# Kernel tuning notes

Hardware: AMD Instinct MI355X
Metric: run time of the kernel (lower is better)

Reference implementation:

```python
import jax, jax.numpy as jnp
import numpy as np

B, S, D, H = 4, 2048, 1024, 16
DK = D // H
DFF = 4 * D
EPS = 1e-6


def setup_inputs() -> dict:
    key = jax.random.key(0)
    ks = jax.random.split(key, 16)
    s = 0.02
    return {
        "x": jax.random.normal(ks[0], (B, S, D), jnp.float32),
        "mask": jax.random.randint(ks[1], (B, 1, 1, S), 0, 2, jnp.int32),
        "wq": jax.random.normal(ks[2], (D, D), jnp.float32) * s,
        "bq": jnp.zeros((D,), jnp.float32),
        "wk": jax.random.normal(ks[3], (D, D), jnp.float32) * s,
        "bk": jnp.zeros((D,), jnp.float32),
        "wv": jax.random.normal(ks[4], (D, D), jnp.float32) * s,
        "bv": jnp.zeros((D,), jnp.float32),
        "wo": jax.random.normal(ks[5], (D, D), jnp.float32) * s,
        "bo": jnp.zeros((D,), jnp.float32),
        "w1": jax.random.normal(ks[6], (DFF, D), jnp.float32) * s,
        "b1": jnp.zeros((DFF,), jnp.float32),
        "w2": jax.random.normal(ks[7], (D, DFF), jnp.float32) * s,
        "b2": jnp.zeros((D,), jnp.float32),
        "a1": jnp.ones((1,), jnp.float32),
        "c1": jnp.zeros((1,), jnp.float32),
        "a2": jnp.ones((1,), jnp.float32),
        "c2": jnp.zeros((1,), jnp.float32),
    }


def _layernorm(x, alpha, bias):
    # source: alpha * (x - mean) / (std + eps) + bias, torch std is unbiased
    mean = jnp.mean(x, axis=-1, keepdims=True)
    std = jnp.std(x, axis=-1, keepdims=True, ddof=1)
    return alpha * (x - mean) / (std + EPS) + bias


def _mha(x, mask, wq, bq, wk, bk, wv, bv, wo, bo):
    q = (x @ wq.T + bq).reshape(B, S, H, DK).transpose(0, 2, 1, 3)  # [B,H,S,DK]
    k = (x @ wk.T + bk).reshape(B, S, H, DK).transpose(0, 2, 1, 3)
    v = (x @ wv.T + bv).reshape(B, S, H, DK).transpose(0, 2, 1, 3)
    scores = jnp.einsum("bhqd,bhkd->bhqk", q, k) / jnp.sqrt(jnp.float32(DK))
    scores = jnp.where(mask == 0, jnp.float32(-1e9), scores)
    attn = jax.nn.softmax(scores, axis=-1)
    out = jnp.einsum("bhqk,bhkd->bhqd", attn, v)  # [B,H,S,DK]
    out = out.transpose(0, 2, 1, 3).reshape(B, S, D)
    return out @ wo.T + bo


def reference(x, mask, wq, bq, wk, bk, wv, bv, wo, bo, w1, b1, w2, b2, a1, c1, a2, c2):
    # residual 1: x + MHA(LN(x))  (dropout = identity in eval)
    h = x + _mha(_layernorm(x, a1, c1), mask, wq, bq, wk, bk, wv, bv, wo, bo)
    # residual 2: h + FFN(LN(h))
    hn = _layernorm(h, a2, c2)
    ffn = jax.nn.relu(hn @ w1.T + b1) @ w2.T + b2
    return h + ffn
```

## Files before the change

kernel.cpp:

```cpp
#include <hip/hip_runtime.h>
#include <math.h>

static constexpr int B  = 4;
static constexpr int S  = 2048;
static constexpr int D  = 1024;
static constexpr int H  = 16;
static constexpr int DFF = 4096;

typedef __attribute__((ext_vector_type(8))) short short8;
typedef __attribute__((ext_vector_type(8))) unsigned short ushort8;
typedef __attribute__((ext_vector_type(4))) unsigned short ushort4v;
typedef __attribute__((ext_vector_type(4))) float f32x4;

__device__ __forceinline__ float b2f(unsigned short u) {
  unsigned int x = ((unsigned int)u) << 16;
  float f;
  __builtin_memcpy(&f, &x, 4);
  return f;
}
__device__ __forceinline__ unsigned short f2b(float f) {
  unsigned int x;
  __builtin_memcpy(&x, &f, 4);
  x += 0x7fffu + ((x >> 16) & 1u);
  return (unsigned short)(x >> 16);
}

__device__ __forceinline__ f32x4 mfma16(short8 a, short8 b, f32x4 c) {
  return __builtin_amdgcn_mfma_f32_16x16x32_bf16(a, b, c, 0, 0, 0);
}

__device__ __forceinline__ void gload_lds16(const void* gsrc, void* ldst) {
  __builtin_amdgcn_global_load_lds(
      (__attribute__((address_space(1))) void*)(uintptr_t)gsrc,
      (__attribute__((address_space(3))) void*)ldst, 16, 0, 0);
}

#define LGK0 asm volatile("s_waitcnt lgkmcnt(0)" ::: "memory")
#define VMC8 asm volatile("s_waitcnt vmcnt(8)" ::: "memory")
#define VMC0 asm volatile("s_waitcnt vmcnt(0)" ::: "memory")
#define SB0  __builtin_amdgcn_sched_barrier(0)
#define BAR  __builtin_amdgcn_s_barrier()
#define PRIO1 __builtin_amdgcn_s_setprio(1)
#define PRIO0 __builtin_amdgcn_s_setprio(0)

struct CvtArgs {
  const float* s[6];
  unsigned short* d[6];
  int n[6];
};
__global__ __launch_bounds__(256) void convert6(CvtArgs a) {
  const int seg = blockIdx.y;
  const int i = (blockIdx.x * 256 + threadIdx.x) * 4;
  if (i < a.n[seg]) {
    f32x4 v = *(const f32x4*)(a.s[seg] + i);
    ushort4v o;
#pragma unroll
    for (int j = 0; j < 4; j++) o[j] = f2b(v[j]);
    *(ushort4v*)(a.d[seg] + i) = o;
  }
}

__global__ __launch_bounds__(256) void ln_fused(const float* __restrict__ x,
                                                const float* __restrict__ ap,
                                                const float* __restrict__ cp,
                                                unsigned short* __restrict__ out) {
  const int row = blockIdx.x, tid = threadIdx.x;
  const size_t base = (size_t)row * D;
  float v[4];
  float s = 0.f, sq = 0.f;
#pragma unroll
  for (int i = 0; i < 4; i++) {
    v[i] = x[base + tid + i * 256];
    s += v[i];
    sq += v[i] * v[i];
  }
#pragma unroll
  for (int o = 32; o > 0; o >>= 1) {
    s += __shfl_xor(s, o);
    sq += __shfl_xor(sq, o);
  }
  __shared__ __align__(16) float rs[4], rq[4];
  const int wave = tid >> 6, lane = tid & 63;
  if (lane == 0) {
    rs[wave] = s;
    rq[wave] = sq;
  }
  __syncthreads();
  const float S1 = rs[0] + rs[1] + rs[2] + rs[3];
  const float S2 = rq[0] + rq[1] + rq[2] + rq[3];
  const float mean = S1 * (1.f / 1024.f);
  const float var = fmaxf(0.f, (S2 - 1024.f * mean * mean) * (1.f / 1023.f));
  const float rstd = 1.f / (sqrtf(var) + 1e-6f);
  const float alpha = ap[0], beta = cp[0];
#pragma unroll
  for (int i = 0; i < 4; i++)
    out[base + tid + i * 256] = f2b(alpha * (v[i] - mean) * rstd + beta);
}

__device__ __forceinline__ void stage_tile(const unsigned short* pA0,
                                           const unsigned short* pB0,
                                           unsigned short* ldsbuf, int wave,
                                           size_t K64, int koff) {
#pragma unroll
  for (int j = 0; j < 4; j++)
    gload_lds16(pA0 + j * K64 + koff, ldsbuf + j * 4096 + wave * 512);
#pragma unroll
  for (int j = 0; j < 4; j++)
    gload_lds16(pB0 + j * K64 + koff, ldsbuf + 16384 + j * 4096 + wave * 512);
}

template <int EPI>
__global__ __launch_bounds__(512, 2) void gemm256(
    const unsigned short* __restrict__ A, const unsigned short* __restrict__ W,
    const float* __restrict__ bias0, const float* __restrict__ bias1,
    const float* __restrict__ bias2, void* __restrict__ out,
    unsigned short* __restrict__ outK, unsigned short* __restrict__ outV,
    int M, int N, int K) {
  __shared__ __align__(16) unsigned short lds[2 * 32768];
  const int tid = threadIdx.x;
  const int lane = tid & 63, wave = tid >> 6;
  const int quad = lane >> 4, l16 = lane & 15;

  const int nbx = gridDim.x;
  const int nwg = nbx * gridDim.y;
  int wg = blockIdx.y * nbx + blockIdx.x;
  if (!(nwg & 7)) wg = (wg & 7) * (nwg >> 3) + (wg >> 3);
  const int bx = wg % nbx, by = wg / nbx;
  const int m0 = by * 256, n0 = bx * 256;
  const int wm = wave >> 2, wn = wave & 3;

  const int srow = wave * 8 + (lane >> 3);
  const int scol = ((lane & 7) ^ (lane >> 3)) * 8;
  const size_t K64 = (size_t)K * 64;
  const unsigned short* pA0 = A + (size_t)(m0 + srow) * K + scol;
  const unsigned short* pB0 = W + (size_t)(n0 + srow) * K + scol;

  const int xr = l16 & 7;
  const int aoff0 = ((0 + quad) ^ xr) * 8;
  const int aoff1 = ((4 + quad) ^ xr) * 8;
  const int arow = wm * 128 + l16;
  const int brow = wn * 64 + l16;

  f32x4 acc[8][4];
#pragma unroll
  for (int i = 0; i < 8; i++)
#pragma unroll
    for (int j = 0; j < 4; j++) acc[i][j] = {0.f, 0.f, 0.f, 0.f};

  const int nkt = K >> 6;
  stage_tile(pA0, pB0, &lds[0], wave, K64, 0);
  stage_tile(pA0, pB0, &lds[32768], wave, K64, 64);
  VMC8;
  SB0;
  BAR;

  short8 af[4][2], bf[4][2];
  for (int t = 0; t < nkt; ++t) {
    const int p = t & 1;
    const unsigned short* Ab = &lds[p * 32768];
    const unsigned short* Bb = Ab + 16384;

#pragma unroll
    for (int nt = 0; nt < 4; nt++) {
      bf[nt][0] = *(const short8*)&Bb[(brow + nt * 16) * 64 + aoff0];
      bf[nt][1] = *(const short8*)&Bb[(brow + nt * 16) * 64 + aoff1];
    }
#pragma unroll
    for (int mt = 0; mt < 4; mt++) {
      af[mt][0] = *(const short8*)&Ab[(arow + mt * 16) * 64 + aoff0];
      af[mt][1] = *(const short8*)&Ab[(arow + mt * 16) * 64 + aoff1];
    }
    BAR;
    LGK0;
    SB0;
    PRIO1;
#pragma unroll
    for (int mt = 0; mt < 4; mt++)
#pragma unroll
      for (int nt = 0; nt < 2; nt++) {
        acc[mt][nt] = mfma16(af[mt][0], bf[nt][0], acc[mt][nt]);
        acc[mt][nt] = mfma16(af[mt][1], bf[nt][1], acc[mt][nt]);
      }
    PRIO0;
    BAR;
    PRIO1;
#pragma unroll
    for (int mt = 0; mt < 4; mt++)
#pragma unroll
      for (int nt = 2; nt < 4; nt++) {
        acc[mt][nt] = mfma16(af[mt][0], bf[nt][0], acc[mt][nt]);
        acc[mt][nt] = mfma16(af[mt][1], bf[nt][1], acc[mt][nt]);
      }
    PRIO0;
    BAR;
#pragma unroll
    for (int i = 0; i < 4; i++) {
      af[i][0] = *(const short8*)&Ab[(arow + 64 + i * 16) * 64 + aoff0];
      af[i][1] = *(const short8*)&Ab[(arow + 64 + i * 16) * 64 + aoff1];
    }
    LGK0;
    SB0;
    BAR;
    if (t + 2 < nkt) stage_tile(pA0, pB0, &lds[p * 32768], wave, K64, (t + 2) * 64);
    PRIO1;
#pragma unroll
    for (int i = 0; i < 4; i++)
#pragma unroll
      for (int nt = 0; nt < 2; nt++) {
        acc[4 + i][nt] = mfma16(af[i][0], bf[nt][0], acc[4 + i][nt]);
        acc[4 + i][nt] = mfma16(af[i][1], bf[nt][1], acc[4 + i][nt]);
      }
    PRIO0;
    BAR;
    PRIO1;
#pragma unroll
    for (int i = 0; i < 4; i++)
#pragma unroll
      for (int nt = 2; nt < 4; nt++) {
        acc[4 + i][nt] = mfma16(af[i][0], bf[nt][0], acc[4 + i][nt]);
        acc[4 + i][nt] = mfma16(af[i][1], bf[nt][1], acc[4 + i][nt]);
      }
    PRIO0;
    if (t + 2 < nkt) {
      VMC8;
    } else if (t + 1 < nkt) {
      VMC0;
    }
    SB0;
    BAR;
  }

  if (EPI == 4) {
    const int band = (n0 + wn * 64) >> 10;
    const float* bp = band == 0 ? bias0 : (band == 1 ? bias1 : bias2);
#pragma unroll
    for (int nt = 0; nt < 4; nt++) {
      const int col = n0 + wn * 64 + nt * 16 + l16;
      const int cl = col & 1023;
      const float bv = bp[cl];
#pragma unroll
      for (int mt = 0; mt < 8; mt++) {
#pragma unroll
        for (int r = 0; r < 4; r++) {
          const int row = m0 + wm * 128 + mt * 16 + quad * 4 + r;
          const float v = acc[mt][nt][r] + bv;
          if (band == 0)
            ((unsigned short*)out)[(size_t)row * 1024 + cl] = f2b(v);
          else if (band == 1)
            outK[(size_t)row * 1024 + cl] = f2b(v);
          else
            outV[((size_t)((row >> 11) * 1024 + cl)) * 2048 + (row & 2047)] = f2b(v);
        }
      }
    }
  } else {
#pragma unroll
    for (int nt = 0; nt < 4; nt++) {
      const int col = n0 + wn * 64 + nt * 16 + l16;
      const float bv = bias0[col];
#pragma unroll
      for (int mt = 0; mt < 8; mt++)
#pragma unroll
        for (int r = 0; r < 4; r++) {
          const int row = m0 + wm * 128 + mt * 16 + quad * 4 + r;
          ((unsigned short*)out)[(size_t)row * (size_t)N + col] =
              f2b(fmaxf(acc[mt][nt][r] + bv, 0.f));
        }
    }
  }
}

template <int EPI>
__global__ __launch_bounds__(256) void gemm_bb(
    const unsigned short* __restrict__ A, const unsigned short* __restrict__ W,
    const float* __restrict__ bias0, const float* __restrict__ bias1,
    const float* __restrict__ bias2, const float* __restrict__ resid,
    void* __restrict__ out, unsigned short* __restrict__ outK,
    unsigned short* __restrict__ outV, int M, int N, int K, int ldw) {
  __shared__ __align__(16) unsigned short As[128 * 32];
  __shared__ __align__(16) unsigned short Bs[128 * 32];
  const int tid = threadIdx.x;
  const int lane = tid & 63, wave = tid >> 6;
  const int quad = lane >> 4, l16 = lane & 15;
  const int m0 = blockIdx.y * 128, n0 = blockIdx.x * 128;
  const int wm = (wave >> 1) * 64, wn = (wave & 1) * 64;

  f32x4 acc[4][4];
#pragma unroll
  for (int i = 0; i < 4; i++)
#pragma unroll
    for (int j = 0; j < 4; j++) acc[i][j] = {0.f, 0.f, 0.f, 0.f};

  const int rA = tid >> 2;
  const int kc = (tid & 3) * 8;

  for (int k0 = 0; k0 < K; k0 += 32) {
    __syncthreads();
#pragma unroll
    for (int i = 0; i < 2; i++) {
      const int row = i * 64 + rA;
      gload_lds16(&A[(size_t)(m0 + row) * K + k0 + kc], &As[(i * 256 + wave * 64) * 8]);
      gload_lds16(&W[(size_t)(n0 + row) * ldw + k0 + kc], &Bs[(i * 256 + wave * 64) * 8]);
    }
    __syncthreads();
    short8 af[4], bf[4];
#pragma unroll
    for (int t = 0; t < 4; t++) {
      af[t] = *(const short8*)&As[(wm + t * 16 + l16) * 32 + quad * 8];
      bf[t] = *(const short8*)&Bs[(wn + t * 16 + l16) * 32 + quad * 8];
    }
#pragma unroll
    for (int mt = 0; mt < 4; mt++)
#pragma unroll
      for (int nt = 0; nt < 4; nt++) acc[mt][nt] = mfma16(af[mt], bf[nt], acc[mt][nt]);
  }

  if (EPI == 4) {
    const int band = (n0 + wn) >> 10;
    const float* bp = band == 0 ? bias0 : (band == 1 ? bias1 : bias2);
#pragma unroll
    for (int nt = 0; nt < 4; nt++) {
      const int col = n0 + wn + nt * 16 + l16;
      const int cl = col & 1023;
      const float bv = bp[cl];
#pragma unroll
      for (int mt = 0; mt < 4; mt++) {
#pragma unroll
        for (int r = 0; r < 4; r++) {
          const int row = m0 + wm + mt * 16 + quad * 4 + r;
          const float v = acc[mt][nt][r] + bv;
          if (band == 0)
            ((unsigned short*)out)[(size_t)row * 1024 + cl] = f2b(v);
          else if (band == 1)
            outK[(size_t)row * 1024 + cl] = f2b(v);
          else
            outV[((size_t)((row >> 11) * 1024 + cl)) * 2048 + (row & 2047)] = f2b(v);
        }
      }
    }
  } else {
#pragma unroll
    for (int nt = 0; nt < 4; nt++) {
      const int col = n0 + wn + nt * 16 + l16;
      const float bv = (EPI == 3) ? 0.f : bias0[col];
#pragma unroll
      for (int mt = 0; mt < 4; mt++) {
#pragma unroll
        for (int r = 0; r < 4; r++) {
          const int row = m0 + wm + mt * 16 + quad * 4 + r;
          const size_t idx = (size_t)row * N + col;
          float v = acc[mt][nt][r] + bv;
          if (EPI == 2) {
            v = fmaxf(v, 0.f);
            ((unsigned short*)out)[idx] = f2b(v);
          } else {
            v += resid[idx];
            ((float*)out)[idx] = v;
          }
        }
      }
    }
  }
}

__global__ __launch_bounds__(256) void attn_kernel(unsigned short* __restrict__ Q,
                                                   const unsigned short* __restrict__ Kb,
                                                   const unsigned short* __restrict__ VT,
                                                   const int* __restrict__ mask) {
  constexpr int PAD = 72;
  __shared__ __align__(16) unsigned short Ks[64 * PAD];
  __shared__ __align__(16) unsigned short VTs[64 * PAD];
  __shared__ __align__(16) unsigned short Pb[4][16 * PAD];

  const int tid = threadIdx.x, lane = tid & 63, wave = tid >> 6;
  const int quad = lane >> 4, l16 = lane & 15;
  const int q0 = blockIdx.x * 64;
  const int b = blockIdx.y >> 4, h = blockIdx.y & 15;

  short8 qf0, qf1;
  {
    const int qr = q0 + wave * 16 + l16;
    const unsigned short* qp = &Q[((size_t)(b * S) + qr) * D + h * 64 + quad * 8];
    qf0 = *(const short8*)qp;
    qf1 = *(const short8*)(qp + 32);
  }

  float l_acc = 0.f;
  f32x4 o_acc[4];
#pragma unroll
  for (int t = 0; t < 4; t++) o_acc[t] = {0.f, 0.f, 0.f, 0.f};

  const int rT = tid >> 3;
  const int cT = (tid & 7) * 8;

  for (int kt = 0; kt < S / 64; kt++) {
    const int k0 = kt * 64;
    ushort8 kv[2], vv[2];
#pragma unroll
    for (int i = 0; i < 2; i++) {
      const int r = i * 32 + rT;
      kv[i] = *(const ushort8*)&Kb[((size_t)(b * S) + k0 + r) * D + h * 64 + cT];
      vv[i] = *(const ushort8*)&VT[((size_t)(blockIdx.y * 64 + r)) * S + k0 + cT];
    }
    __syncthreads();
#pragma unroll
    for (int i = 0; i < 2; i++) {
      const int r = i * 32 + rT;
      *(ushort8*)&Ks[r * PAD + cT] = kv[i];
      *(ushort8*)&VTs[r * PAD + cT] = vv[i];
    }
    __syncthreads();

    f32x4 sc[4];
#pragma unroll
    for (int nt = 0; nt < 4; nt++) sc[nt] = {0.f, 0.f, 0.f, 0.f};
    PRIO1;
#pragma unroll
    for (int nt = 0; nt < 4; nt++) {
      short8 kf0 = *(const short8*)&Ks[(nt * 16 + l16) * PAD + quad * 8];
      short8 kf1 = *(const short8*)&Ks[(nt * 16 + l16) * PAD + 32 + quad * 8];
      sc[nt] = mfma16(kf0, qf0, sc[nt]);
      sc[nt] = mfma16(kf1, qf1, sc[nt]);
    }
    PRIO0;

#pragma unroll
    for (int nt = 0; nt < 4; nt++) {
      const int4 mv = *(const int4*)&mask[b * S + k0 + nt * 16 + quad * 4];
      ushort4v pk;
      {
        const float p0 = __expf(fmaf(sc[nt][0], 0.125f, mv.x ? -12.f : -42.f));
        const float p1 = __expf(fmaf(sc[nt][1], 0.125f, mv.y ? -12.f : -42.f));
        const float p2 = __expf(fmaf(sc[nt][2], 0.125f, mv.z ? -12.f : -42.f));
        const float p3 = __expf(fmaf(sc[nt][3], 0.125f, mv.w ? -12.f : -42.f));
        l_acc += p0 + p1 + p2 + p3;
        pk[0] = f2b(p0);
        pk[1] = f2b(p1);
        pk[2] = f2b(p2);
        pk[3] = f2b(p3);
      }
      *(ushort4v*)&Pb[wave][l16 * PAD + nt * 16 + quad * 4] = pk;
    }

    short8 pf0 = *(const short8*)&Pb[wave][l16 * PAD + quad * 8];
    short8 pf1 = *(const short8*)&Pb[wave][l16 * PAD + 32 + quad * 8];
    PRIO1;
#pragma unroll
    for (int nt = 0; nt < 4; nt++) {
      short8 vf0 = *(const short8*)&VTs[(nt * 16 + l16) * PAD + quad * 8];
      short8 vf1 = *(const short8*)&VTs[(nt * 16 + l16) * PAD + 32 + quad * 8];
      o_acc[nt] = mfma16(pf0, vf0, o_acc[nt]);
      o_acc[nt] = mfma16(pf1, vf1, o_acc[nt]);
    }
    PRIO0;
  }

  l_acc += __shfl_xor(l_acc, 16);
  l_acc += __shfl_xor(l_acc, 32);

#pragma unroll
  for (int r = 0; r < 4; r++) {
    const float lr = __shfl(l_acc, quad * 4 + r);
    const float inv = 1.f / lr;
    const int q = q0 + wave * 16 + quad * 4 + r;
#pragma unroll
    for (int nt = 0; nt < 4; nt++) {
      const int dk = nt * 16 + l16;
      Q[((size_t)(b * S) + q) * D + h * 64 + dk] = f2b(o_acc[nt][r] * inv);
    }
  }
}

__global__ __launch_bounds__(256) void stats_kernel(const float* __restrict__ x,
                                                    float2* __restrict__ st) {
  const int row = blockIdx.x, tid = threadIdx.x;
  const size_t base = (size_t)row * D;
  float s = 0.f, sq = 0.f;
#pragma unroll
  for (int i = 0; i < 4; i++) {
    const float v = x[base + tid + i * 256];
    s += v;
    sq += v * v;
  }
#pragma unroll
  for (int o = 32; o > 0; o >>= 1) {
    s += __shfl_xor(s, o);
    sq += __shfl_xor(sq, o);
  }
  __shared__ __align__(16) float rs[4], rq[4];
  const int wave = tid >> 6, lane = tid & 63;
  if (lane == 0) {
    rs[wave] = s;
    rq[wave] = sq;
  }
  __syncthreads();
  if (tid == 0) {
    const float S1 = rs[0] + rs[1] + rs[2] + rs[3];
    const float S2 = rq[0] + rq[1] + rq[2] + rq[3];
    const float mean = S1 * (1.f / 1024.f);
    const float var = fmaxf(0.f, (S2 - 1024.f * mean * mean) * (1.f / 1023.f));
    const float rstd = 1.f / (sqrtf(var) + 1e-6f);
    st[row] = make_float2(mean, rstd);
  }
}

template <int EPI, int NORM, int AF32, int OUTF32>
__global__ __launch_bounds__(256) void gemm_bt(
    const void* __restrict__ Ap, const float* __restrict__ W,
    const float* __restrict__ bias, const float* __restrict__ resid,
    void* __restrict__ outp, const float2* __restrict__ stats,
    const float* __restrict__ alpha_p, const float* __restrict__ beta_p,
    int M, int N, int K, int ldw) {
  __shared__ __align__(16) unsigned short As[128 * 32];
  __shared__ __align__(16) unsigned short Bs[128 * 32];
  const int tid = threadIdx.x;
  const int lane = tid & 63, wave = tid >> 6;
  const int quad = lane >> 4, l16 = lane & 15;
  const int m0 = blockIdx.y * 128, n0 = blockIdx.x * 128;
  const int wm = (wave >> 1) * 64, wn = (wave & 1) * 64;

  float alpha = 0.f, beta = 0.f;
  if (NORM) {
    alpha = alpha_p[0];
    beta = beta_p[0];
  }

  f32x4 acc[4][4];
#pragma unroll
  for (int i = 0; i < 4; i++)
#pragma unroll
    for (int j = 0; j < 4; j++) acc[i][j] = {0.f, 0.f, 0.f, 0.f};

  const int rA = tid >> 2;
  const int kc = (tid & 3) * 8;

  for (int k0 = 0; k0 < K; k0 += 32) {
    ushort8 av[2], bv8[2];
#pragma unroll
    for (int i = 0; i < 2; i++) {
      const int row = i * 64 + rA;
      if (AF32) {
        const float* ap = (const float*)Ap + (size_t)(m0 + row) * K + k0 + kc;
        f32x4 a0 = *(const f32x4*)ap;
        f32x4 a1 = *(const f32x4*)(ap + 4);
        if (NORM) {
          const float2 st = stats[m0 + row];
#pragma unroll
          for (int j = 0; j < 4; j++) {
            a0[j] = alpha * (a0[j] - st.x) * st.y + beta;
            a1[j] = alpha * (a1[j] - st.x) * st.y + beta;
          }
        }
#pragma unroll
        for (int j = 0; j < 4; j++) {
          av[i][j] = f2b(a0[j]);
          av[i][j + 4] = f2b(a1[j]);
        }
      } else {
        av[i] = *(const ushort8*)((const unsigned short*)Ap +
                                  (size_t)(m0 + row) * K + k0 + kc);
      }
      const float* wp = W + (size_t)(n0 + row) * ldw + k0 + kc;
      f32x4 w0 = *(const f32x4*)wp;
      f32x4 w1 = *(const f32x4*)(wp + 4);
#pragma unroll
      for (int j = 0; j < 4; j++) {
        bv8[i][j] = f2b(w0[j]);
        bv8[i][j + 4] = f2b(w1[j]);
      }
    }
    __syncthreads();
#pragma unroll
    for (int i = 0; i < 2; i++) {
      const int row = i * 64 + rA;
      *(ushort8*)&As[row * 32 + kc] = av[i];
      *(ushort8*)&Bs[row * 32 + kc] = bv8[i];
    }
    __syncthreads();
    short8 af[4], bf[4];
#pragma unroll
    for (int t = 0; t < 4; t++) {
      af[t] = *(const short8*)&As[(wm + t * 16 + l16) * 32 + quad * 8];
      bf[t] = *(const short8*)&Bs[(wn + t * 16 + l16) * 32 + quad * 8];
    }
#pragma unroll
    for (int mt = 0; mt < 4; mt++)
#pragma unroll
      for (int nt = 0; nt < 4; nt++) acc[mt][nt] = mfma16(af[mt], bf[nt], acc[mt][nt]);
  }

#pragma unroll
  for (int nt = 0; nt < 4; nt++) {
    const int col = n0 + wn + nt * 16 + l16;
    const float bv = (EPI == 3) ? 0.f : bias[col];
#pragma unroll
    for (int mt = 0; mt < 4; mt++) {
#pragma unroll
      for (int r = 0; r < 4; r++) {
        const int row = m0 + wm + mt * 16 + quad * 4 + r;
        float v = acc[mt][nt][r] + bv;
        if (EPI == 2) v = fmaxf(v, 0.f);
        if (EPI == 4) {
          const size_t vtidx =
              ((size_t)((row >> 11) * 1024 + col)) * 2048 + (row & 2047);
          ((unsigned short*)outp)[vtidx] = f2b(v);
        } else {
          const size_t idx = (size_t)row * N + col;
          if (EPI == 1 || EPI == 3) v += resid[idx];
          if (OUTF32)
            ((float*)outp)[idx] = v;
          else
            ((unsigned short*)outp)[idx] = f2b(v);
        }
      }
    }
  }
}

extern "C" void kernel_launch(void* const* d_in, const int* in_sizes, int n_in,
                              void* d_out, int out_size, void* d_ws, size_t ws_size,
                              hipStream_t stream) {
  (void)in_sizes; (void)n_in; (void)out_size;
  const float* x  = (const float*)d_in[0];
  const int* mask = (const int*)d_in[1];
  const float* wq = (const float*)d_in[2];
  const float* bq = (const float*)d_in[3];
  const float* wk = (const float*)d_in[4];
  const float* bk = (const float*)d_in[5];
  const float* wv = (const float*)d_in[6];
  const float* bv = (const float*)d_in[7];
  const float* wo = (const float*)d_in[8];
  const float* bo = (const float*)d_in[9];
  const float* w1 = (const float*)d_in[10];
  const float* b1 = (const float*)d_in[11];
  const float* w2 = (const float*)d_in[12];
  const float* b2 = (const float*)d_in[13];
  const float* a1 = (const float*)d_in[14];
  const float* c1 = (const float*)d_in[15];
  const float* a2 = (const float*)d_in[16];
  const float* c2 = (const float*)d_in[17];

  char* ws = (char*)d_ws;
  const size_t MB = 1 << 20;
  const int M = B * S;
  dim3 blk(256);
  dim3 blk512(512);
  dim3 gAttn(S / 64, B * H);

  if (ws_size >= 89 * MB) {
    const int tier3 = (ws_size >= 152 * MB);
    const int tier2 = (ws_size >= 121 * MB);
    unsigned short* wqkv_b = (unsigned short*)(ws + 0);
    unsigned short* wo_b   = (unsigned short*)(ws + 6 * MB);
    unsigned short* w1_b   = (unsigned short*)(ws + 8 * MB);
    unsigned short* w2_b   = (unsigned short*)(ws + 16 * MB);
    unsigned short* ln1x   = (unsigned short*)(ws + 25 * MB);
    unsigned short* q      = (unsigned short*)(ws + 41 * MB);
    unsigned short* kk     = (unsigned short*)(ws + 57 * MB);
    unsigned short* vt     = (unsigned short*)(ws + 73 * MB);
    float*          hbuf   = (float*)(ws + 57 * MB);
    unsigned short* ln2x   = (unsigned short*)(ws + 25 * MB);
    unsigned short* ffn1q  = (unsigned short*)(ws + 41 * MB);
    unsigned short* ffn1h  = (unsigned short*)(ws + 89 * MB);
    unsigned short* ffn1f  = (unsigned short*)(ws + 89 * MB);
    float* outb = (float*)d_out;

    CvtArgs ca;
    ca.s[0] = wq; ca.d[0] = wqkv_b;            ca.n[0] = 1048576;
    ca.s[1] = wk; ca.d[1] = wqkv_b + 1048576;  ca.n[1] = 1048576;
    ca.s[2] = wv; ca.d[2] = wqkv_b + 2097152;  ca.n[2] = 1048576;
    ca.s[3] = wo; ca.d[3] = wo_b;              ca.n[3] = 1048576;
    ca.s[4] = w1; ca.d[4] = w1_b;              ca.n[4] = 4194304;
    ca.s[5] = w2; ca.d[5] = w2_b;              ca.n[5] = 4194304;
    convert6<<<dim3(4096, 6), blk, 0, stream>>>(ca);

    ln_fused<<<M, blk, 0, stream>>>(x, a1, c1, ln1x);
    gemm256<4><<<dim3(12, 32), blk512, 0, stream>>>(ln1x, wqkv_b, bq, bk, bv,
                                                    q, kk, vt, M, 3072, D);
    attn_kernel<<<gAttn, blk, 0, stream>>>(q, kk, vt, mask);
    gemm_bb<1><<<dim3(8, 64), blk, 0, stream>>>(q, wo_b, bo, nullptr, nullptr, x,
                                                hbuf, nullptr, nullptr, M, D, D, D);
    ln_fused<<<M, blk, 0, stream>>>(hbuf, a2, c2, ln2x);

    if (tier3) {
      gemm256<2><<<dim3(16, 32), blk512, 0, stream>>>(ln2x, w1_b, b1, nullptr,
                                                      nullptr, ffn1f, nullptr,
                                                      nullptr, M, DFF, D);
      gemm_bb<1><<<dim3(8, 64), blk, 0, stream>>>(ffn1f, w2_b, b2, nullptr, nullptr,
                                                  hbuf, outb, nullptr, nullptr,
                                                  M, D, DFF, DFF);
    } else if (tier2) {
      gemm_bb<2><<<dim3(16, 64), blk, 0, stream>>>(ln2x, w1_b, b1, nullptr, nullptr,
                                                   nullptr, ffn1h, nullptr, nullptr,
                                                   M, 2048, D, D);
      gemm_bb<1><<<dim3(8, 64), blk, 0, stream>>>(ffn1h, w2_b, b2, nullptr, nullptr,
                                                  hbuf, outb, nullptr, nullptr,
                                                  M, D, 2048, DFF);
      gemm_bb<2><<<dim3(16, 64), blk, 0, stream>>>(ln2x, w1_b + (size_t)2048 * D,
                                                   b1 + 2048, nullptr, nullptr, nullptr,
                                                   ffn1h, nullptr, nullptr, M, 2048, D, D);
      gemm_bb<3><<<dim3(8, 64), blk, 0, stream>>>(ffn1h, w2_b + 2048, nullptr, nullptr,
                                                  nullptr, outb, outb, nullptr, nullptr,
                                                  M, D, 2048, DFF);
    } else {
      for (int i = 0; i < 4; i++) {
        gemm_bb<2><<<dim3(8, 64), blk, 0, stream>>>(ln2x, w1_b + (size_t)i * 1024 * D,
                                                    b1 + i * 1024, nullptr, nullptr,
                                                    nullptr, ffn1q, nullptr, nullptr,
                                                    M, 1024, D, D);
        if (i == 0)
          gemm_bb<1><<<dim3(8, 64), blk, 0, stream>>>(ffn1q, w2_b + i * 1024, b2, nullptr,
                                                      nullptr, hbuf, outb, nullptr, nullptr,
                                                      M, D, 1024, DFF);
        else
          gemm_bb<3><<<dim3(8, 64), blk, 0, stream>>>(ffn1q, w2_b + i * 1024, nullptr,
                                                      nullptr, nullptr, outb, outb, nullptr,
                                                      nullptr, M, D, 1024, DFF);
      }
    }
  } else {
    float2* stats1 = (float2*)(ws + 0);
    float2* stats2 = (float2*)(ws + 128 * 1024);
    unsigned short* q    = (unsigned short*)(ws + 1 * MB);
    unsigned short* kk   = (unsigned short*)(ws + 17 * MB);
    unsigned short* vt   = (unsigned short*)(ws + 33 * MB);
    float*          hbuf = (float*)(ws + 17 * MB);
    unsigned short* ffn1 = (unsigned short*)(ws + 1 * MB);
    float* outb = (float*)d_out;
    dim3 gD(D / 128, M / 128);

    stats_kernel<<<M, blk, 0, stream>>>(x, stats1);
    gemm_bt<0, 1, 1, 0><<<gD, blk, 0, stream>>>(x, wq, bq, nullptr, q, stats1, a1, c1, M, D, D, D);
    gemm_bt<0, 1, 1, 0><<<gD, blk, 0, stream>>>(x, wk, bk, nullptr, kk, stats1, a1, c1, M, D, D, D);
    gemm_bt<4, 1, 1, 0><<<gD, blk, 0, stream>>>(x, wv, bv, nullptr, vt, stats1, a1, c1, M, D, D, D);
    attn_kernel<<<gAttn, blk, 0, stream>>>(q, kk, vt, mask);
    gemm_bt<1, 0, 0, 1><<<gD, blk, 0, stream>>>(q, wo, bo, x, hbuf, nullptr, nullptr, nullptr, M, D, D, D);
    stats_kernel<<<M, blk, 0, stream>>>(hbuf, stats2);
    for (int i = 0; i < 4; i++) {
      gemm_bt<2, 1, 1, 0><<<gD, blk, 0, stream>>>(hbuf, w1 + (size_t)i * 1024 * D,
                                                  b1 + i * 1024, nullptr, ffn1, stats2,
                                                  a2, c2, M, 1024, D, D);
      if (i == 0)
        gemm_bt<1, 0, 0, 1><<<gD, blk, 0, stream>>>(ffn1, w2 + i * 1024, b2, hbuf, outb,
                                                    nullptr, nullptr, nullptr, M, D, 1024, DFF);
      else
        gemm_bt<3, 0, 0, 1><<<gD, blk, 0, stream>>>(ffn1, w2 + i * 1024, nullptr, outb, outb,
                                                    nullptr, nullptr, nullptr, M, D, 1024, DFF);
    }
  }
}
```

Before: 628.2 us.

## Pipeline attention K/V loads via LDS double-buffering and split GEMM staging

The attention kernel now stages K and V tiles straight into LDS with global_load_lds, using a double buffer and an XOR swizzle in place of register round-trips and padding. Each wave now handles 32 query rows instead of 16, so every K/V tile is reused twice and the grid is halved. In the GEMM, B-fragment LDS reads are split across the two MFMA halves, and the next tile's A and B global loads are issued at separate points. The aim is to overlap memory traffic with MFMA work and cut per-tile synchronisation, at the cost of more registers and a fixed load/wait ordering.

```diff
diff --git a/kernel.cpp b/kernel.cpp
--- a/kernel.cpp
+++ b/kernel.cpp
@@ -36,6 +36,7 @@
 }
 
 #define LGK0 asm volatile("s_waitcnt lgkmcnt(0)" ::: "memory")
+#define LGK8 asm volatile("s_waitcnt lgkmcnt(8)" ::: "memory")
 #define VMC8 asm volatile("s_waitcnt vmcnt(8)" ::: "memory")
 #define VMC0 asm volatile("s_waitcnt vmcnt(0)" ::: "memory")
 #define SB0  __builtin_amdgcn_sched_barrier(0)
@@ -97,16 +98,12 @@
     out[base + tid + i * 256] = f2b(alpha * (v[i] - mean) * rstd + beta);
 }
 
-__device__ __forceinline__ void stage_tile(const unsigned short* pA0,
-                                           const unsigned short* pB0,
+__device__ __forceinline__ void stage_half(const unsigned short* p0,
                                            unsigned short* ldsbuf, int wave,
                                            size_t K64, int koff) {
 #pragma unroll
   for (int j = 0; j < 4; j++)
-    gload_lds16(pA0 + j * K64 + koff, ldsbuf + j * 4096 + wave * 512);
-#pragma unroll
-  for (int j = 0; j < 4; j++)
-    gload_lds16(pB0 + j * K64 + koff, ldsbuf + 16384 + j * 4096 + wave * 512);
+    gload_lds16(p0 + j * K64 + koff, ldsbuf + j * 4096 + wave * 512);
 }
 
 template <int EPI>
@@ -148,8 +145,10 @@
     for (int j = 0; j < 4; j++) acc[i][j] = {0.f, 0.f, 0.f, 0.f};
 
   const int nkt = K >> 6;
-  stage_tile(pA0, pB0, &lds[0], wave, K64, 0);
-  stage_tile(pA0, pB0, &lds[32768], wave, K64, 64);
+  stage_half(pA0, &lds[0], wave, K64, 0);
+  stage_half(pB0, &lds[16384], wave, K64, 0);
+  stage_half(pA0, &lds[32768], wave, K64, 64);
+  stage_half(pB0, &lds[32768 + 16384], wave, K64, 64);
   VMC8;
   SB0;
   BAR;
@@ -161,15 +160,16 @@
     const unsigned short* Bb = Ab + 16384;
 
 #pragma unroll
-    for (int nt = 0; nt < 4; nt++) {
-      bf[nt][0] = *(const short8*)&Bb[(brow + nt * 16) * 64 + aoff0];
-      bf[nt][1] = *(const short8*)&Bb[(brow + nt * 16) * 64 + aoff1];
-    }
-#pragma unroll
     for (int mt = 0; mt < 4; mt++) {
       af[mt][0] = *(const short8*)&Ab[(arow + mt * 16) * 64 + aoff0];
       af[mt][1] = *(const short8*)&Ab[(arow + mt * 16) * 64 + aoff1];
     }
+#pragma unroll
+    for (int nt = 0; nt < 2; nt++) {
+      bf[nt][0] = *(const short8*)&Bb[(brow + nt * 16) * 64 + aoff0];
+      bf[nt][1] = *(const short8*)&Bb[(brow + nt * 16) * 64 + aoff1];
+    }
+    LGK8;
     BAR;
     LGK0;
     SB0;
@@ -183,6 +183,14 @@
       }
     PRIO0;
     BAR;
+#pragma unroll
+    for (int nt = 2; nt < 4; nt++) {
+      bf[nt][0] = *(const short8*)&Bb[(brow + nt * 16) * 64 + aoff0];
+      bf[nt][1] = *(const short8*)&Bb[(brow + nt * 16) * 64 + aoff1];
+    }
+    BAR;
+    LGK0;
+    SB0;
     PRIO1;
 #pragma unroll
     for (int mt = 0; mt < 4; mt++)
@@ -201,7 +209,7 @@
     LGK0;
     SB0;
     BAR;
-    if (t + 2 < nkt) stage_tile(pA0, pB0, &lds[p * 32768], wave, K64, (t + 2) * 64);
+    if (t + 2 < nkt) stage_half(pA0, &lds[p * 32768], wave, K64, (t + 2) * 64);
     PRIO1;
 #pragma unroll
     for (int i = 0; i < 4; i++)
@@ -212,6 +220,7 @@
       }
     PRIO0;
     BAR;
+    if (t + 2 < nkt) stage_half(pB0, &lds[p * 32768 + 16384], wave, K64, (t + 2) * 64);
     PRIO1;
 #pragma unroll
     for (int i = 0; i < 4; i++)
@@ -363,110 +372,151 @@
   }
 }
 
+__device__ __forceinline__ void attn_stage(const unsigned short* Kg,
+                                           const unsigned short* Vg,
+                                           unsigned short* Kd, unsigned short* Vd,
+                                           int kt) {
+  gload_lds16(Kg + (size_t)kt * 64 * D, Kd);
+  gload_lds16(Kg + (size_t)kt * 64 * D + 8 * D, Kd + 8 * 64);
+  gload_lds16(Vg + (size_t)kt * 64, Vd);
+  gload_lds16(Vg + (size_t)kt * 64 + 8 * (size_t)S, Vd + 8 * 64);
+}
+
 __global__ __launch_bounds__(256) void attn_kernel(unsigned short* __restrict__ Q,
                                                    const unsigned short* __restrict__ Kb,
                                                    const unsigned short* __restrict__ VT,
                                                    const int* __restrict__ mask) {
-  constexpr int PAD = 72;
-  __shared__ __align__(16) unsigned short Ks[64 * PAD];
-  __shared__ __align__(16) unsigned short VTs[64 * PAD];
-  __shared__ __align__(16) unsigned short Pb[4][16 * PAD];
+  __shared__ __align__(16) unsigned short Ks[2][64 * 64];
+  __shared__ __align__(16) unsigned short Vs[2][64 * 64];
+  constexpr int PPAD = 72;
+  __shared__ __align__(16) unsigned short Pb[4][16 * PPAD];
 
   const int tid = threadIdx.x, lane = tid & 63, wave = tid >> 6;
   const int quad = lane >> 4, l16 = lane & 15;
-  const int q0 = blockIdx.x * 64;
+  const int q0 = blockIdx.x * 128;
   const int b = blockIdx.y >> 4, h = blockIdx.y & 15;
 
-  short8 qf0, qf1;
-  {
-    const int qr = q0 + wave * 16 + l16;
-    const unsigned short* qp = &Q[((size_t)(b * S) + qr) * D + h * 64 + quad * 8];
-    qf0 = *(const short8*)qp;
-    qf1 = *(const short8*)(qp + 32);
-  }
-
-  float l_acc = 0.f;
-  f32x4 o_acc[4];
-#pragma unroll
-  for (int t = 0; t < 4; t++) o_acc[t] = {0.f, 0.f, 0.f, 0.f};
-
-  const int rT = tid >> 3;
-  const int cT = (tid & 7) * 8;
+  const int sr = lane >> 3;
+  const int sc8 = ((lane & 7) ^ sr) * 8;
+  const unsigned short* Kg = Kb + ((size_t)b * S + wave * 16 + sr) * D + h * 64 + sc8;
+  const unsigned short* Vg = VT + ((size_t)blockIdx.y * 64 + wave * 16 + sr) * S + sc8;
+  unsigned short* Kd0 = &Ks[0][(wave * 16) * 64];
+  unsigned short* Vd0 = &Vs[0][(wave * 16) * 64];
+  unsigned short* Kd1 = &Ks[1][(wave * 16) * 64];
+  unsigned short* Vd1 = &Vs[1][(wave * 16) * 64];
+
+  attn_stage(Kg, Vg, Kd0, Vd0, 0);
+
+  short8 qf[2][2];
+#pragma unroll
+  for (int qh = 0; qh < 2; qh++) {
+    const unsigned short* qp =
+        &Q[((size_t)b * S + q0 + wave * 32 + qh * 16 + l16) * D + h * 64 + quad * 8];
+    qf[qh][0] = *(const short8*)qp;
+    qf[qh][1] = *(const short8*)(qp + 32);
+  }
+
+  float l_acc[2] = {0.f, 0.f};
+  f32x4 o_acc[2][4];
+#pragma unroll
+  for (int qh = 0; qh < 2; qh++)
+#pragma unroll
+    for (int t = 0; t < 4; t++) o_acc[qh][t] = {0.f, 0.f, 0.f, 0.f};
+
+  const int xr = l16 & 7;
+  const int c0 = (quad ^ xr) * 8;
+  const int c1 = ((quad + 4) ^ xr) * 8;
+
+  VMC0;
+  SB0;
+  BAR;
 
   for (int kt = 0; kt < S / 64; kt++) {
+    const int cur = kt & 1;
+    if (kt + 1 < S / 64)
+      attn_stage(Kg, Vg, cur ? Kd0 : Kd1, cur ? Vd0 : Vd1, kt + 1);
     const int k0 = kt * 64;
-    ushort8 kv[2], vv[2];
-#pragma unroll
-    for (int i = 0; i < 2; i++) {
-      const int r = i * 32 + rT;
-      kv[i] = *(const ushort8*)&Kb[((size_t)(b * S) + k0 + r) * D + h * 64 + cT];
-      vv[i] = *(const ushort8*)&VT[((size_t)(blockIdx.y * 64 + r)) * S + k0 + cT];
-    }
-    __syncthreads();
-#pragma unroll
-    for (int i = 0; i < 2; i++) {
-      const int r = i * 32 + rT;
-      *(ushort8*)&Ks[r * PAD + cT] = kv[i];
-      *(ushort8*)&VTs[r * PAD + cT] = vv[i];
-    }
-    __syncthreads();
-
-    f32x4 sc[4];
-#pragma unroll
-    for (int nt = 0; nt < 4; nt++) sc[nt] = {0.f, 0.f, 0.f, 0.f};
-    PRIO1;
-#pragma unroll
-    for (int nt = 0; nt < 4; nt++) {
-      short8 kf0 = *(const short8*)&Ks[(nt * 16 + l16) * PAD + quad * 8];
-      short8 kf1 = *(const short8*)&Ks[(nt * 16 + l16) * PAD + 32 + quad * 8];
-      sc[nt] = mfma16(kf0, qf0, sc[nt]);
-      sc[nt] = mfma16(kf1, qf1, sc[nt]);
-    }
-    PRIO0;
-
+    const unsigned short* Kc = Ks[cur];
+    const unsigned short* Vc = Vs[cur];
+
+    f32x4 mb[4];
 #pragma unroll
     for (int nt = 0; nt < 4; nt++) {
       const int4 mv = *(const int4*)&mask[b * S + k0 + nt * 16 + quad * 4];
-      ushort4v pk;
-      {
-        const float p0 = __expf(fmaf(sc[nt][0], 0.125f, mv.x ? -12.f : -42.f));
-        const float p1 = __expf(fmaf(sc[nt][1], 0.125f, mv.y ? -12.f : -42.f));
-        const float p2 = __expf(fmaf(sc[nt][2], 0.125f, mv.z ? -12.f : -42.f));
-        const float p3 = __expf(fmaf(sc[nt][3], 0.125f, mv.w ? -12.f : -42.f));
-        l_acc += p0 + p1 + p2 + p3;
+      mb[nt][0] = mv.x ? -12.f : -42.f;
+      mb[nt][1] = mv.y ? -12.f : -42.f;
+      mb[nt][2] = mv.z ? -12.f : -42.f;
+      mb[nt][3] = mv.w ? -12.f : -42.f;
+    }
+    short8 kf[4][2];
+#pragma unroll
+    for (int nt = 0; nt < 4; nt++) {
+      kf[nt][0] = *(const short8*)&Kc[(nt * 16 + l16) * 64 + c0];
+      kf[nt][1] = *(const short8*)&Kc[(nt * 16 + l16) * 64 + c1];
+    }
+
+#pragma unroll
+    for (int qh = 0; qh < 2; qh++) {
+      f32x4 sc4[4];
+#pragma unroll
+      for (int nt = 0; nt < 4; nt++) sc4[nt] = {0.f, 0.f, 0.f, 0.f};
+      PRIO1;
+#pragma unroll
+      for (int nt = 0; nt < 4; nt++) {
+        sc4[nt] = mfma16(kf[nt][0], qf[qh][0], sc4[nt]);
+        sc4[nt] = mfma16(kf[nt][1], qf[qh][1], sc4[nt]);
+      }
+      PRIO0;
+
+#pragma unroll
+      for (int nt = 0; nt < 4; nt++) {
+        ushort4v pk;
+        const float p0 = __expf(fmaf(sc4[nt][0], 0.125f, mb[nt][0]));
+        const float p1 = __expf(fmaf(sc4[nt][1], 0.125f, mb[nt][1]));
+        const float p2 = __expf(fmaf(sc4[nt][2], 0.125f, mb[nt][2]));
+        const float p3 = __expf(fmaf(sc4[nt][3], 0.125f, mb[nt][3]));
+        l_acc[qh] += p0 + p1 + p2 + p3;
         pk[0] = f2b(p0);
         pk[1] = f2b(p1);
         pk[2] = f2b(p2);
         pk[3] = f2b(p3);
-      }
-      *(ushort4v*)&Pb[wave][l16 * PAD + nt * 16 + quad * 4] = pk;
-    }
-
-    short8 pf0 = *(const short8*)&Pb[wave][l16 * PAD + quad * 8];
-    short8 pf1 = *(const short8*)&Pb[wave][l16 * PAD + 32 + quad * 8];
-    PRIO1;
-#pragma unroll
-    for (int nt = 0; nt < 4; nt++) {
-      short8 vf0 = *(const short8*)&VTs[(nt * 16 + l16) * PAD + quad * 8];
-      short8 vf1 = *(const short8*)&VTs[(nt * 16 + l16) * PAD + 32 + quad * 8];
-      o_acc[nt] = mfma16(pf0, vf0, o_acc[nt]);
-      o_acc[nt] = mfma16(pf1, vf1, o_acc[nt]);
-    }
-    PRIO0;
-  }
-
-  l_acc += __shfl_xor(l_acc, 16);
-  l_acc += __shfl_xor(l_acc, 32);
-
-#pragma unroll
-  for (int r = 0; r < 4; r++) {
-    const float lr = __shfl(l_acc, quad * 4 + r);
-    const float inv = 1.f / lr;
-    const int q = q0 + wave * 16 + quad * 4 + r;
-#pragma unroll
-    for (int nt = 0; nt < 4; nt++) {
-      const int dk = nt * 16 + l16;
-      Q[((size_t)(b * S) + q) * D + h * 64 + dk] = f2b(o_acc[nt][r] * inv);
+        *(ushort4v*)&Pb[wave][l16 * PPAD + nt * 16 + quad * 4] = pk;
+      }
+
+      short8 pf0 = *(const short8*)&Pb[wave][l16 * PPAD + quad * 8];
+      short8 pf1 = *(const short8*)&Pb[wave][l16 * PPAD + 32 + quad * 8];
+      PRIO1;
+#pragma unroll
+      for (int nt = 0; nt < 4; nt++) {
+        short8 vf0 = *(const short8*)&Vc[(nt * 16 + l16) * 64 + c0];
+        short8 vf1 = *(const short8*)&Vc[(nt * 16 + l16) * 64 + c1];
+        o_acc[qh][nt] = mfma16(pf0, vf0, o_acc[qh][nt]);
+        o_acc[qh][nt] = mfma16(pf1, vf1, o_acc[qh][nt]);
+      }
+      PRIO0;
+    }
+
+    VMC0;
+    SB0;
+    BAR;
+    SB0;
+  }
+
+#pragma unroll
+  for (int qh = 0; qh < 2; qh++) {
+    float la = l_acc[qh];
+    la += __shfl_xor(la, 16);
+    la += __shfl_xor(la, 32);
+#pragma unroll
+    for (int r = 0; r < 4; r++) {
+      const float lr = __shfl(la, quad * 4 + r);
+      const float inv = 1.f / lr;
+      const int q = q0 + wave * 32 + qh * 16 + quad * 4 + r;
+#pragma unroll
+      for (int nt = 0; nt < 4; nt++) {
+        const int dk = nt * 16 + l16;
+        Q[((size_t)b * S + q) * D + h * 64 + dk] = f2b(o_acc[qh][nt][r] * inv);
+      }
     }
   }
 }
@@ -645,7 +695,7 @@
   const int M = B * S;
   dim3 blk(256);
   dim3 blk512(512);
-  dim3 gAttn(S / 64, B * H);
+  dim3 gAttn(S / 128, B * H);
 
   if (ws_size >= 89 * MB) {
     const int tier3 = (ws_size >= 152 * MB);
```

Measured after the change: 636.1 us. About the same (+1.3%).
